# Optimization experiments

Measured on AMD Instinct MI355X. Metric: run time of the kernel, lower is better.

## Reference

```python
import jax, jax.numpy as jnp
import numpy as np

N = 576        # variable nodes (from filename wman_N0576)
MROWS = 144    # check nodes = N*(1 - 3/4)
ROW_DEG = 15   # check-node degree (WiMAX rate-3/4 style)
BATCH = 256
ITERS = 3


def _make_H():
    # deterministic binary parity-check matrix with fixed row degree >= 2
    rng = np.random.default_rng(0)
    cols = np.argsort(rng.random((MROWS, N)), axis=1)[:, :ROW_DEG]
    H = np.zeros((MROWS, N), dtype=np.float32)
    H[np.arange(MROWS)[:, None], cols] = 1.0
    return jnp.asarray(H)


def setup_inputs() -> dict:
    key = jax.random.key(0)
    r = jax.random.normal(key, (BATCH, N), dtype=jnp.float32)  # channel LLRs
    alpha = jnp.full((ITERS,), 0.7, dtype=jnp.float32)
    beta = jnp.full((ITERS,), 0.05, dtype=jnp.float32)
    return {"r": r, "H": _make_H(), "alpha": alpha, "beta": beta}


def _c_to_v(M, H, node_idx, alpha, beta):
    # min-sum check-to-variable messages with offset beta and scale alpha
    abs_M = jnp.abs(M)                                   # [B, MROWS, N]
    masked = jnp.where(H == 1.0, abs_M, jnp.inf)
    neg_top, idx = jax.lax.top_k(-masked, 2)             # two smallest per row
    min1 = -neg_top[..., 0:1]
    min2 = -neg_top[..., 1:2]
    idx1 = idx[..., 0:1]
    E_abs = jnp.where(node_idx == idx1, min2, min1)      # exclude-self min
    valid = jnp.where(H == 1.0, jnp.sign(M), 1.0)
    row_prod = jnp.prod(valid, axis=2, keepdims=True)    # total sign per check
    E_sign = row_prod * valid                            # exclude-self sign
    E = alpha * E_sign * jnp.maximum(0.0, E_abs - beta)
    return E * H


def reference(r, H, alpha, beta):
    node_idx = jnp.arange(N)[None, None, :]              # [1,1,N]
    M = H[None, :, :] * r[:, None, :]                    # initial v->c messages
    E = jnp.zeros_like(M)
    for it in range(ITERS):
        E = _c_to_v(M, H, node_idx, alpha[it], beta[it])
        sum_E = jnp.sum(E, axis=1, keepdims=True)        # [B,1,N]
        M = (r[:, None, :] + sum_E - E) * H[None, :, :]
    return r + jnp.sum(E, axis=1)                        # posterior LLRs [B,N]
```

## Files before the change

### kernel.cpp

```cpp
#include <hip/hip_runtime.h>

#define NVAR   576
#define NROW   144
#define DEG    15
#define NEDGE  (NROW * DEG)
#define NBATCH 256
#define NITER  3
#define NT     576
#define EPT    4

__global__ void build_cols_kernel(const float* __restrict__ H,
                                  short* __restrict__ cols) {
    int gid  = blockIdx.x * blockDim.x + threadIdx.x;
    int wid  = gid >> 6;
    int lane = gid & 63;
    if (wid >= NROW) return;
    const float* Hr = H + wid * NVAR;
    int base = 0;
    #pragma unroll
    for (int c = 0; c < NVAR / 64; ++c) {
        float h = Hr[c * 64 + lane];
        unsigned long long m = __ballot(h != 0.0f);
        int rank = __popcll(m & ((1ull << lane) - 1ull));
        if (h != 0.0f) cols[wid * DEG + base + rank] = (short)(c * 64 + lane);
        base += __popcll(m);
    }
}

__launch_bounds__(NT, 1)
__global__ void ldpc_minsum_kernel(const float* __restrict__ r,
                                   const short* __restrict__ cols_g,
                                   const float* __restrict__ alpha,
                                   const float* __restrict__ beta,
                                   float* __restrict__ out) {
    __shared__ float  rs[NVAR];
    __shared__ float  sumE[NVAR];
    __shared__ float  rnew[NVAR];
    __shared__ short  cols[NEDGE];
    __shared__ float  Msh[NEDGE];
    __shared__ float4 rowdat[NROW];

    const int b = blockIdx.x;
    const int t = threadIdx.x;

    float alr[NITER], ber[NITER];
    #pragma unroll
    for (int i = 0; i < NITER; ++i) { alr[i] = alpha[i]; ber[i] = beta[i]; }

    rs[t] = r[b * NVAR + t];
    #pragma unroll
    for (int k = 0; k < EPT; ++k) {
        int e = t + k * NT;
        if (e < NEDGE) cols[e] = cols_g[e];
    }
    __syncthreads();

    int ec[EPT], em[EPT], ej[EPT];
    float mv[EPT], ev[EPT];
    #pragma unroll
    for (int k = 0; k < EPT; ++k) {
        int e = t + k * NT;
        if (e < NEDGE) {
            int c = cols[e];
            int m = e / DEG;
            ec[k] = c; em[k] = m; ej[k] = e - m * DEG;
            float v = rs[c];
            mv[k] = v;
            Msh[e] = v;
        }
    }
    __syncthreads();

    #pragma unroll
    for (int it = 0; it < NITER; ++it) {
        if (t < NROW) {
            float m1 = INFINITY, m2 = INFINITY, sg = 1.0f;
            int j1 = 0;
            const float* Mr = &Msh[t * DEG];
            #pragma unroll
            for (int j = 0; j < DEG; ++j) {
                float v = Mr[j];
                float a = fabsf(v);
                float s = (v > 0.0f) ? 1.0f : ((v < 0.0f) ? -1.0f : 0.0f);
                sg *= s;
                if (a < m1) { m2 = m1; m1 = a; j1 = j; }
                else if (a < m2) { m2 = a; }
            }
            rowdat[t] = make_float4(m1, m2, sg, __int_as_float(j1));
        }
        sumE[t] = 0.0f;
        __syncthreads();

        #pragma unroll
        for (int k = 0; k < EPT; ++k) {
            int e = t + k * NT;
            if (e < NEDGE) {
                float v = mv[k];
                float4 rd = rowdat[em[k]];
                float s = (v > 0.0f) ? 1.0f : ((v < 0.0f) ? -1.0f : 0.0f);
                float eabs = (ej[k] == __float_as_int(rd.w)) ? rd.y : rd.x;
                float e_ = alr[it] * rd.z * s * fmaxf(0.0f, eabs - ber[it]);
                ev[k] = e_;
                atomicAdd(&sumE[ec[k]], e_);
            }
        }
        __syncthreads();

        float v = rs[t] + sumE[t];
        if (it == NITER - 1) {
            out[b * NVAR + t] = v;
        } else {
            rnew[t] = v;
            __syncthreads();
            #pragma unroll
            for (int k = 0; k < EPT; ++k) {
                int e = t + k * NT;
                if (e < NEDGE) {
                    float nv = rnew[ec[k]] - ev[k];
                    mv[k] = nv;
                    Msh[e] = nv;
                }
            }
            __syncthreads();
        }
    }
}

extern "C" void kernel_launch(void* const* d_in, const int* in_sizes, int n_in,
                              void* d_out, int out_size, void* d_ws, size_t ws_size,
                              hipStream_t stream) {
    const float* r     = (const float*)d_in[0];
    const float* H     = (const float*)d_in[1];
    const float* alpha = (const float*)d_in[2];
    const float* beta  = (const float*)d_in[3];
    float* out  = (float*)d_out;
    short* cols = (short*)d_ws;

    build_cols_kernel<<<36, 256, 0, stream>>>(H, cols);
    ldpc_minsum_kernel<<<NBATCH, NT, 0, stream>>>(r, cols, alpha, beta, out);
}
```

Before: 77.93 us.

## Process each check row per thread in registers, double-buffer sumE

Reassigns work so each of 144 threads owns one check row and keeps its 15 messages, column indices and extrinsic values in registers, and shrinks the block to 192 threads. Edge messages are no longer staged in shared memory and row min data is not broadcast, and ping-pong sum buffers remove one barrier per iteration. The cost is less parallelism per block (only 144 active threads in the compute phase, so several waves sit idle), more registers per thread, and serialized atomics within each thread.

```diff
diff --git a/kernel.cpp b/kernel.cpp
--- a/kernel.cpp
+++ b/kernel.cpp
@@ -6,8 +6,7 @@
 #define NEDGE  (NROW * DEG)
 #define NBATCH 256
 #define NITER  3
-#define NT     576
-#define EPT    4
+#define NT     192
 
 __global__ void build_cols_kernel(const float* __restrict__ H,
                                   short* __restrict__ cols) {
@@ -33,12 +32,9 @@
                                    const float* __restrict__ alpha,
                                    const float* __restrict__ beta,
                                    float* __restrict__ out) {
-    __shared__ float  rs[NVAR];
-    __shared__ float  sumE[NVAR];
-    __shared__ float  rnew[NVAR];
-    __shared__ short  cols[NEDGE];
-    __shared__ float  Msh[NEDGE];
-    __shared__ float4 rowdat[NROW];
+    __shared__ float rs[NVAR];
+    __shared__ float sA[NVAR];
+    __shared__ float sB[NVAR];
 
     const int b = blockIdx.x;
     const int t = threadIdx.x;
@@ -47,79 +43,65 @@
     #pragma unroll
     for (int i = 0; i < NITER; ++i) { alr[i] = alpha[i]; ber[i] = beta[i]; }
 
-    rs[t] = r[b * NVAR + t];
     #pragma unroll
-    for (int k = 0; k < EPT; ++k) {
-        int e = t + k * NT;
-        if (e < NEDGE) cols[e] = cols_g[e];
+    for (int k = 0; k < 3; ++k) {
+        int n = t + k * NT;
+        rs[n] = r[b * NVAR + n];
+        sA[n] = 0.0f;
     }
     __syncthreads();
 
-    int ec[EPT], em[EPT], ej[EPT];
-    float mv[EPT], ev[EPT];
-    #pragma unroll
-    for (int k = 0; k < EPT; ++k) {
-        int e = t + k * NT;
-        if (e < NEDGE) {
-            int c = cols[e];
-            int m = e / DEG;
-            ec[k] = c; em[k] = m; ej[k] = e - m * DEG;
-            float v = rs[c];
-            mv[k] = v;
-            Msh[e] = v;
-        }
+    int   ci[DEG];
+    float Mv[DEG], Ev[DEG], rc[DEG];
+    if (t < NROW) {
+        #pragma unroll
+        for (int j = 0; j < DEG; ++j) ci[j] = (int)cols_g[t * DEG + j];
+        #pragma unroll
+        for (int j = 0; j < DEG; ++j) { rc[j] = rs[ci[j]]; Mv[j] = rc[j]; }
     }
-    __syncthreads();
 
     #pragma unroll
     for (int it = 0; it < NITER; ++it) {
+        float* sum = (it & 1) ? sB : sA;
+        float* nxt = (it & 1) ? sA : sB;
+
         if (t < NROW) {
             float m1 = INFINITY, m2 = INFINITY, sg = 1.0f;
             int j1 = 0;
-            const float* Mr = &Msh[t * DEG];
             #pragma unroll
             for (int j = 0; j < DEG; ++j) {
-                float v = Mr[j];
+                float v = Mv[j];
                 float a = fabsf(v);
                 float s = (v > 0.0f) ? 1.0f : ((v < 0.0f) ? -1.0f : 0.0f);
                 sg *= s;
                 if (a < m1) { m2 = m1; m1 = a; j1 = j; }
                 else if (a < m2) { m2 = a; }
             }
-            rowdat[t] = make_float4(m1, m2, sg, __int_as_float(j1));
-        }
-        sumE[t] = 0.0f;
-        __syncthreads();
-
-        #pragma unroll
-        for (int k = 0; k < EPT; ++k) {
-            int e = t + k * NT;
-            if (e < NEDGE) {
-                float v = mv[k];
-                float4 rd = rowdat[em[k]];
+            #pragma unroll
+            for (int j = 0; j < DEG; ++j) {
+                float v = Mv[j];
                 float s = (v > 0.0f) ? 1.0f : ((v < 0.0f) ? -1.0f : 0.0f);
-                float eabs = (ej[k] == __float_as_int(rd.w)) ? rd.y : rd.x;
-                float e_ = alr[it] * rd.z * s * fmaxf(0.0f, eabs - ber[it]);
-                ev[k] = e_;
-                atomicAdd(&sumE[ec[k]], e_);
+                float eabs = (j == j1) ? m2 : m1;
+                float e = alr[it] * sg * s * fmaxf(0.0f, eabs - ber[it]);
+                Ev[j] = e;
+                atomicAdd(&sum[ci[j]], e);
             }
         }
         __syncthreads();
 
-        float v = rs[t] + sumE[t];
         if (it == NITER - 1) {
-            out[b * NVAR + t] = v;
+            #pragma unroll
+            for (int k = 0; k < 3; ++k) {
+                int n = t + k * NT;
+                out[b * NVAR + n] = rs[n] + sum[n];
+            }
         } else {
-            rnew[t] = v;
-            __syncthreads();
             #pragma unroll
-            for (int k = 0; k < EPT; ++k) {
-                int e = t + k * NT;
-                if (e < NEDGE) {
-                    float nv = rnew[ec[k]] - ev[k];
-                    mv[k] = nv;
-                    Msh[e] = nv;
-                }
+            for (int k = 0; k < 3; ++k) nxt[t + k * NT] = 0.0f;
+            if (t < NROW) {
+                #pragma unroll
+                for (int j = 0; j < DEG; ++j)
+                    Mv[j] = rc[j] + sum[ci[j]] - Ev[j];
             }
             __syncthreads();
         }
```

New measurement: 75.13 us. 1.04x faster.
